# Performance work log

Hardware: AMD Instinct MI355X
Metric: run time of the kernel (lower is better)

Reference implementation:

```python
import jax, jax.numpy as jnp
import numpy as np

HIDDEN = 2048
NUM_HEADS = 16
HEAD_DIM = HIDDEN // NUM_HEADS  # 128
LAYER_IDX = 0


def setup_inputs() -> dict:
    key = jax.random.key(0)
    k1, k2, k3, k4, k5 = jax.random.split(key, 5)
    B, S = 2, 2048
    hidden_states = jax.random.normal(k1, (B, S, HIDDEN), dtype=jnp.float32)
    # causal mask, broadcastable to attn shape (B, Q, H, K)
    causal = jnp.tril(jnp.ones((S, S), dtype=jnp.bool_))  # [Q, K]
    attention_mask = causal[None, :, None, :]  # [1, Q, 1, K]
    c_attn_w = jax.random.normal(k2, (HIDDEN, HIDDEN + 2 * HEAD_DIM), dtype=jnp.float32) * 0.02
    c_attn_b = jax.random.normal(k3, (HIDDEN + 2 * HEAD_DIM,), dtype=jnp.float32) * 0.02
    c_proj_w = jax.random.normal(k4, (HIDDEN, HIDDEN), dtype=jnp.float32) * 0.02
    c_proj_b = jax.random.normal(k5, (HIDDEN,), dtype=jnp.float32) * 0.02
    return {
        "hidden_states": hidden_states,
        "attention_mask": attention_mask,
        "c_attn_w": c_attn_w,
        "c_attn_b": c_attn_b,
        "c_proj_w": c_proj_w,
        "c_proj_b": c_proj_b,
    }


def reference(hidden_states, attention_mask, c_attn_w, c_attn_b, c_proj_w, c_proj_b):
    B, S, D = hidden_states.shape
    H, hd = NUM_HEADS, HEAD_DIM
    # c_attn then split into per-head query and shared (MQA) key/value
    qkv = hidden_states @ c_attn_w + c_attn_b  # [B, S, D + 2*hd]
    query = qkv[..., :D].reshape(B, S, H, hd)  # [B, Q, H, hd]
    k = qkv[..., D:D + hd]                     # [B, K, hd] shared across heads
    v = qkv[..., D + hd:]                      # [B, K, hd]
    # fp32 input => upcast=False => unscale=1, scale = 1/sqrt(head_dim)
    scale = 1.0 / jnp.sqrt(jnp.float32(hd))
    scores = jnp.einsum('bqhd,bkd->bqhk', query, k) * scale  # [B, Q, H, K]
    mask_value = jnp.finfo(jnp.float32).min
    scores = jnp.where(attention_mask, scores, mask_value)
    attn = jax.nn.softmax(scores, axis=-1)
    attn_output = jnp.einsum('bqhk,bkd->bqhd', attn, v).reshape(B, S, D)
    attn_output = attn_output @ c_proj_w + c_proj_b
    return attn_output
```

## Files before the change

### kernel.cpp

```cpp
#include <hip/hip_runtime.h>
#include <hip/hip_bf16.h>

typedef __bf16 bf16_t;
typedef __bf16 bf16x8 __attribute__((ext_vector_type(8)));
typedef __bf16 bf16x4 __attribute__((ext_vector_type(4)));
typedef float f32x4 __attribute__((ext_vector_type(4)));

#define S_LEN 2048
#define HID   2048
#define NH    16
#define HD    128
#define QKVN  2304
#define NEG_BIG (-30000.0f)
#define RESCALE_THR 8.0f

__device__ __forceinline__ void gld_lds16(const bf16_t* g, bf16_t* l) {
  __builtin_amdgcn_global_load_lds(
      (const __attribute__((address_space(1))) void*)((const void*)g),
      (__attribute__((address_space(3))) void*)((void*)l), 16, 0, 0);
}

__global__ __launch_bounds__(256) void cvt_f32_bf16_kernel(
    const float* __restrict__ in, bf16_t* __restrict__ out, int n)
{
  int i = (blockIdx.x * 256 + threadIdx.x) * 4;
  if (i < n) {
    float4 v = *(const float4*)(in + i);
    bf16x4 o;
    o[0] = (bf16_t)v.x; o[1] = (bf16_t)v.y; o[2] = (bf16_t)v.z; o[3] = (bf16_t)v.w;
    *(bf16x4*)(out + i) = o;
  }
}

__global__ __launch_bounds__(256) void transpose_cvt_kernel(
    const float* __restrict__ in, bf16_t* __restrict__ out, int K, int N)
{
  int nc = threadIdx.x & 63;
  int kg = threadIdx.x >> 6;
  int n  = blockIdx.x * 64 + nc;
  int kb = blockIdx.y * 32 + kg * 8;
  bf16x8 v;
  #pragma unroll
  for (int i = 0; i < 8; ++i) v[i] = (bf16_t)in[(size_t)(kb + i) * N + n];
  *(bf16x8*)(out + (size_t)n * K + kb) = v;
}

__global__ __launch_bounds__(256) void vt_extract_kernel(
    const bf16_t* __restrict__ qkv, bf16_t* __restrict__ vtg)
{
  int d  = threadIdx.x & 127;
  int sg = threadIdx.x >> 7;
  int b  = blockIdx.y;
  int s8 = blockIdx.x * 2 + sg;
  bf16x8 v;
  #pragma unroll
  for (int i = 0; i < 8; ++i)
    v[i] = qkv[((size_t)(b * S_LEN + s8 * 8 + i)) * QKVN + HID + HD + d];
  *(bf16x8*)(vtg + ((size_t)(b * HD + d)) * S_LEN + s8 * 8) = v;
}

template <typename OutT>
__global__ __launch_bounds__(512, 4) void gemm_bias_kernel(
    const bf16_t* __restrict__ A, const bf16_t* __restrict__ WT,
    const float* __restrict__ bias, OutT* __restrict__ C,
    int K, int lda, int ldc)
{
  __shared__ bf16_t Ash[2 * 128 * 64];
  __shared__ bf16_t Bsh[2 * 128 * 64];

  const int tid  = threadIdx.x;
  const int wave = tid >> 6;
  const int lane = tid & 63;
  const int quad = lane >> 4;
  const int c16  = lane & 15;
  const int wm = wave >> 2;
  const int wn = wave & 3;

  int id  = (int)(blockIdx.y * gridDim.x + blockIdx.x);
  int nwg = (int)(gridDim.x * gridDim.y);
  int swz = (nwg & 7) ? id : ((id & 7) * (nwg >> 3) + (id >> 3));
  const int n0 = (swz % (int)gridDim.x) * 128;
  const int m0 = (swz / (int)gridDim.x) * 128;

  f32x4 acc[4][2] = {};

  #define GSTAGE(bufi, k0v) do {                                             \
    bf16_t* Ad_ = Ash + (bufi) * 8192;                                       \
    bf16_t* Bd_ = Bsh + (bufi) * 8192;                                       \
    _Pragma("unroll")                                                        \
    for (int j_ = 0; j_ < 2; ++j_) {                                         \
      int cbase_ = wave * 128 + j_ * 64;                                     \
      int c_ = cbase_ + lane;                                                \
      int row_ = c_ >> 3;                                                    \
      int kcl_ = (c_ ^ row_) & 7;                                            \
      gld_lds16(A  + (size_t)(m0 + row_) * lda + (k0v) + kcl_ * 8,           \
                Ad_ + cbase_ * 8);                                           \
      gld_lds16(WT + (size_t)(n0 + row_) * K   + (k0v) + kcl_ * 8,           \
                Bd_ + cbase_ * 8);                                           \
    }                                                                        \
  } while (0)

  GSTAGE(0, 0);
  int cur = 0;

  for (int k0 = 0; k0 < K; k0 += 64) {
    __syncthreads();
    if (k0 + 64 < K) GSTAGE(cur ^ 1, k0 + 64);

    const bf16_t* Ac = Ash + cur * 8192;
    const bf16_t* Bc = Bsh + cur * 8192;
    #pragma unroll
    for (int kk = 0; kk < 2; ++kk) {
      bf16x8 af[4], bfr[2];
      #pragma unroll
      for (int rb = 0; rb < 4; ++rb) {
        int row = wm * 64 + rb * 16 + c16;
        int kcp = ((kk * 4 + quad) ^ row) & 7;
        af[rb] = *(const bf16x8*)(Ac + row * 64 + kcp * 8);
      }
      #pragma unroll
      for (int nt = 0; nt < 2; ++nt) {
        int row = wn * 32 + nt * 16 + c16;
        int kcp = ((kk * 4 + quad) ^ row) & 7;
        bfr[nt] = *(const bf16x8*)(Bc + row * 64 + kcp * 8);
      }
      #pragma unroll
      for (int rb = 0; rb < 4; ++rb)
        #pragma unroll
        for (int nt = 0; nt < 2; ++nt)
          acc[rb][nt] = __builtin_amdgcn_mfma_f32_16x16x32_bf16(af[rb], bfr[nt],
                                                                acc[rb][nt], 0, 0, 0);
    }
    cur ^= 1;
  }
  #undef GSTAGE

  #pragma unroll
  for (int nt = 0; nt < 2; ++nt) {
    int col = n0 + wn * 32 + nt * 16 + c16;
    float bv = bias[col];
    #pragma unroll
    for (int rb = 0; rb < 4; ++rb) {
      int rbase = m0 + wm * 64 + rb * 16 + quad * 4;
      #pragma unroll
      for (int r = 0; r < 4; ++r)
        C[(size_t)(rbase + r) * ldc + col] = (OutT)(acc[rb][nt][r] + bv);
    }
  }
}

__global__ __launch_bounds__(512, 4) void mqa_attn_kernel(
    const bf16_t* __restrict__ qkv, const bf16_t* __restrict__ vtg,
    bf16_t* __restrict__ out)
{
  __shared__ bf16_t sh[40960];

  const int tid  = threadIdx.x;
  const int wv   = tid >> 6;
  const int lane = tid & 63;
  const int quad = lane >> 4;
  const int c16  = lane & 15;
  const int h = blockIdx.y;
  const int b = blockIdx.z;
  const float qscale = 0.08838834764831845f * 1.4426950408889634f;

  const bf16_t* kbase = qkv + (size_t)b * S_LEN * QKVN + HID;
  const bf16_t* vtb   = vtg + (size_t)b * HD * S_LEN;

  const int qh = ((int)blockIdx.x + h) & 15;
  const int Q  = b ? (15 - qh) : qh;
  const int q0 = Q * 128;
  const int qrow = q0 + wv * 16 + c16;
  const int ntile = 2 * Q + 2;

  const bf16_t* qp = qkv + ((size_t)(b * S_LEN + qrow)) * QKVN + h * HD;
  bf16x8 qf[4];
  #pragma unroll
  for (int ks = 0; ks < 4; ++ks) {
    bf16x8 t = *(const bf16x8*)(qp + ks * 32 + quad * 8);
    #pragma unroll
    for (int j = 0; j < 8; ++j) t[j] = (bf16_t)((float)t[j] * qscale);
    qf[ks] = t;
  }

  float m_q = NEG_BIG, l_q = 0.0f;
  f32x4 o[8] = {};

  const int prow = wv * 16 + c16;
  const int rsw  = prow & 7;
  bf16_t* Pbase = sh + 32768 + (size_t)prow * 64;

  #define STAGE(bufi, kti) do {                                              \
    const bf16_t* kb_ = kbase + (size_t)(kti) * 64 * QKVN;                   \
    const bf16_t* vb_ = vtb + (kti) * 64;                                    \
    bf16_t* Kd_ = sh + (bufi) * 8192;                                        \
    bf16_t* Vd_ = sh + 16384 + (bufi) * 8192;                                \
    _Pragma("unroll")                                                        \
    for (int i_ = 0; i_ < 2; ++i_) {                                         \
      int c_ = tid + i_ * 512;                                               \
      int r_ = c_ >> 4, lc_ = (c_ & 15) ^ (r_ & 7);                          \
      gld_lds16(kb_ + (size_t)r_ * QKVN + lc_ * 8, Kd_ + (c_ & ~63) * 8);    \
    }                                                                        \
    _Pragma("unroll")                                                        \
    for (int i_ = 0; i_ < 2; ++i_) {                                         \
      int c_ = tid + i_ * 512;                                               \
      int r_ = c_ >> 3, lc_ = (c_ & 7) ^ (r_ & 7);                           \
      gld_lds16(vb_ + (size_t)r_ * S_LEN + lc_ * 8, Vd_ + (c_ & ~63) * 8);   \
    }                                                                        \
  } while (0)

  STAGE(0, 0);
  int cur = 0;

  for (int kt = 0; kt < ntile; ++kt) {
    __syncthreads();
    if (kt + 1 < ntile) STAGE(cur ^ 1, kt + 1);

    const bf16_t* Kc = sh + cur * 8192;
    const bf16_t* Vc = sh + 16384 + cur * 8192;
    const bool wactive = (kt * 64) <= (q0 + wv * 16 + 15);
    if (wactive) {
      f32x4 sacc[4] = {};
      __builtin_amdgcn_s_setprio(1);
      #pragma unroll
      for (int mt = 0; mt < 4; ++mt) {
        int krow = mt * 16 + c16;
        #pragma unroll
        for (int ks = 0; ks < 4; ++ks) {
          bf16x8 kf = *(const bf16x8*)(Kc + krow * 128 +
                                       (((ks * 4 + quad) ^ (krow & 7)) << 3));
          sacc[mt] = __builtin_amdgcn_mfma_f32_16x16x32_bf16(kf, qf[ks], sacc[mt], 0, 0, 0);
        }
      }
      __builtin_amdgcn_s_setprio(0);

      float mx = NEG_BIG;
      if (kt * 64 + 63 > q0 + wv * 16) {
        #pragma unroll
        for (int mt = 0; mt < 4; ++mt) {
          #pragma unroll
          for (int r = 0; r < 4; ++r) {
            int key = kt * 64 + mt * 16 + quad * 4 + r;
            float v = sacc[mt][r];
            if (key > qrow) v = NEG_BIG;
            sacc[mt][r] = v;
            mx = fmaxf(mx, v);
          }
        }
      } else {
        #pragma unroll
        for (int mt = 0; mt < 4; ++mt) {
          #pragma unroll
          for (int r = 0; r < 4; ++r) mx = fmaxf(mx, sacc[mt][r]);
        }
      }
      mx = fmaxf(mx, __shfl_xor(mx, 16));
      mx = fmaxf(mx, __shfl_xor(mx, 32));

      if (__any(mx > m_q + RESCALE_THR)) {
        float mn = fmaxf(m_q, mx);
        float alpha = __builtin_exp2f(m_q - mn);
        m_q = mn;
        l_q *= alpha;
        #pragma unroll
        for (int mt8 = 0; mt8 < 8; ++mt8) {
          #pragma unroll
          for (int r = 0; r < 4; ++r) o[mt8][r] *= alpha;
        }
      }

      float rs = 0.f;
      #pragma unroll
      for (int mt = 0; mt < 4; ++mt) {
        #pragma unroll
        for (int r = 0; r < 4; ++r) {
          float pe = __builtin_exp2f(sacc[mt][r] - m_q);
          sacc[mt][r] = pe;
          rs += pe;
        }
      }
      rs += __shfl_xor(rs, 16);
      rs += __shfl_xor(rs, 32);
      l_q += rs;

      #pragma unroll
      for (int mt = 0; mt < 4; ++mt) {
        bf16x4 pk;
        #pragma unroll
        for (int r = 0; r < 4; ++r) pk[r] = (bf16_t)sacc[mt][r];
        int ch = 2 * mt + (quad >> 1);
        *(bf16x4*)(Pbase + (((ch ^ rsw) << 3) + (quad & 1) * 4)) = pk;
      }
      bf16x8 pf[2];
      #pragma unroll
      for (int kh = 0; kh < 2; ++kh)
        pf[kh] = *(const bf16x8*)(Pbase + (((4 * kh + quad) ^ rsw) << 3));

      __builtin_amdgcn_s_setprio(1);
      #pragma unroll
      for (int mt8 = 0; mt8 < 8; ++mt8) {
        int vrow = mt8 * 16 + c16;
        #pragma unroll
        for (int kh = 0; kh < 2; ++kh) {
          bf16x8 vf = *(const bf16x8*)(Vc + vrow * 64 +
                                       (((kh * 4 + quad) ^ (vrow & 7)) << 3));
          o[mt8] = __builtin_amdgcn_mfma_f32_16x16x32_bf16(vf, pf[kh], o[mt8], 0, 0, 0);
        }
      }
      __builtin_amdgcn_s_setprio(0);
    }
    cur ^= 1;
  }
  #undef STAGE

  __syncthreads();
  float inv = 1.0f / fmaxf(l_q, 1e-20f);
  bf16_t* Osh = sh;
  #pragma unroll
  for (int mt8 = 0; mt8 < 8; ++mt8) {
    bf16x4 pk;
    #pragma unroll
    for (int r = 0; r < 4; ++r) pk[r] = (bf16_t)(o[mt8][r] * inv);
    *(bf16x4*)(&Osh[(size_t)prow * 136 + mt8 * 16 + quad * 4]) = pk;
  }
  int ql = lane >> 2, dc = lane & 3;
  #pragma unroll
  for (int i = 0; i < 4; ++i) {
    bf16x8 v = *(const bf16x8*)(&Osh[(size_t)(wv * 16 + ql) * 136 + dc * 8 + i * 32]);
    *(bf16x8*)(out + ((size_t)(b * S_LEN + q0 + wv * 16 + ql)) * HID
                   + h * HD + dc * 8 + i * 32) = v;
  }
}

extern "C" void kernel_launch(void* const* d_in, const int* in_sizes, int n_in,
                              void* d_out, int out_size, void* d_ws, size_t ws_size,
                              hipStream_t stream) {
  const float* hidden_f   = (const float*)d_in[0];
  const float* c_attn_w_f = (const float*)d_in[2];
  const float* c_attn_b_f = (const float*)d_in[3];
  const float* c_proj_w_f = (const float*)d_in[4];
  const float* c_proj_b_f = (const float*)d_in[5];
  float* out = (float*)d_out;

  const int M = 2 * S_LEN;
  const int nH  = M * HID;
  const int nWq = HID * QKVN;
  const int nWp = HID * HID;

  bf16_t* hbf   = (bf16_t*)d_ws;
  bf16_t* wqT   = hbf  + nH;
  bf16_t* wpT   = wqT  + nWq;
  bf16_t* qkv   = wpT  + nWp;
  bf16_t* attn  = qkv  + (size_t)M * QKVN;
  bf16_t* vtg   = attn + (size_t)M * HID;

  cvt_f32_bf16_kernel<<<nH / 1024, 256, 0, stream>>>(hidden_f, hbf, nH);
  dim3 gt1(QKVN / 64, HID / 32);
  transpose_cvt_kernel<<<gt1, 256, 0, stream>>>(c_attn_w_f, wqT, HID, QKVN);
  dim3 gt2(HID / 64, HID / 32);
  transpose_cvt_kernel<<<gt2, 256, 0, stream>>>(c_proj_w_f, wpT, HID, HID);

  dim3 g1(QKVN / 128, M / 128);
  gemm_bias_kernel<bf16_t><<<g1, 512, 0, stream>>>(hbf, wqT, c_attn_b_f, qkv,
                                                   HID, HID, QKVN);

  dim3 gv(S_LEN / 16, 2);
  vt_extract_kernel<<<gv, 256, 0, stream>>>(qkv, vtg);

  dim3 g2(16, NH, 2);
  mqa_attn_kernel<<<g2, 512, 0, stream>>>(qkv, vtg, attn);

  dim3 g3(HID / 128, M / 128);
  gemm_bias_kernel<float><<<g3, 512, 0, stream>>>(attn, wpT, c_proj_b_f, out,
                                                  HID, HID, HID);
}
```

Baseline: 300.4 us.

## Merge prep conversions into one kernel and emit V-transpose from QKV GEMM epilogue

```diff
diff --git a/kernel.cpp b/kernel.cpp
--- a/kernel.cpp
+++ b/kernel.cpp
@@ -20,50 +20,47 @@
       (__attribute__((address_space(3))) void*)((void*)l), 16, 0, 0);
 }
 
-__global__ __launch_bounds__(256) void cvt_f32_bf16_kernel(
-    const float* __restrict__ in, bf16_t* __restrict__ out, int n)
+__device__ __forceinline__ void transpose_cvt_body(
+    const float* __restrict__ in, bf16_t* __restrict__ out,
+    int K, int N, int bx, int by, int tid)
 {
-  int i = (blockIdx.x * 256 + threadIdx.x) * 4;
-  if (i < n) {
-    float4 v = *(const float4*)(in + i);
+  int nc = tid & 63;
+  int kg = tid >> 6;
+  int n  = bx * 64 + nc;
+  int kb = by * 32 + kg * 8;
+  bf16x8 v;
+  #pragma unroll
+  for (int i = 0; i < 8; ++i) v[i] = (bf16_t)in[(size_t)(kb + i) * N + n];
+  *(bf16x8*)(out + (size_t)n * K + kb) = v;
+}
+
+__global__ __launch_bounds__(256) void prep_kernel(
+    const float* __restrict__ hidden, bf16_t* __restrict__ hbf,
+    const float* __restrict__ wq, bf16_t* __restrict__ wqT,
+    const float* __restrict__ wp, bf16_t* __restrict__ wpT)
+{
+  const int id  = blockIdx.x;
+  const int tid = threadIdx.x;
+  if (id < 8192) {
+    int i = (id * 256 + tid) * 4;
+    float4 v = *(const float4*)(hidden + i);
     bf16x4 o;
     o[0] = (bf16_t)v.x; o[1] = (bf16_t)v.y; o[2] = (bf16_t)v.z; o[3] = (bf16_t)v.w;
-    *(bf16x4*)(out + i) = o;
-  }
-}
-
-__global__ __launch_bounds__(256) void transpose_cvt_kernel(
-    const float* __restrict__ in, bf16_t* __restrict__ out, int K, int N)
-{
-  int nc = threadIdx.x & 63;
-  int kg = threadIdx.x >> 6;
-  int n  = blockIdx.x * 64 + nc;
-  int kb = blockIdx.y * 32 + kg * 8;
-  bf16x8 v;
-  #pragma unroll
-  for (int i = 0; i < 8; ++i) v[i] = (bf16_t)in[(size_t)(kb + i) * N + n];
-  *(bf16x8*)(out + (size_t)n * K + kb) = v;
-}
-
-__global__ __launch_bounds__(256) void vt_extract_kernel(
-    const bf16_t* __restrict__ qkv, bf16_t* __restrict__ vtg)
-{
-  int d  = threadIdx.x & 127;
-  int sg = threadIdx.x >> 7;
-  int b  = blockIdx.y;
-  int s8 = blockIdx.x * 2 + sg;
-  bf16x8 v;
-  #pragma unroll
-  for (int i = 0; i < 8; ++i)
-    v[i] = qkv[((size_t)(b * S_LEN + s8 * 8 + i)) * QKVN + HID + HD + d];
-  *(bf16x8*)(vtg + ((size_t)(b * HD + d)) * S_LEN + s8 * 8) = v;
+    *(bf16x4*)(hbf + i) = o;
+  } else if (id < 8192 + 2304) {
+    int id2 = id - 8192;
+    transpose_cvt_body(wq, wqT, HID, QKVN, id2 % 36, id2 / 36, tid);
+  } else {
+    int id2 = id - 10496;
+    transpose_cvt_body(wp, wpT, HID, HID, id2 % 32, id2 / 32, tid);
+  }
 }
 
 template <typename OutT>
 __global__ __launch_bounds__(512, 4) void gemm_bias_kernel(
     const bf16_t* __restrict__ A, const bf16_t* __restrict__ WT,
     const float* __restrict__ bias, OutT* __restrict__ C,
-    int K, int lda, int ldc)
+    bf16_t* __restrict__ vt_out, int K, int lda, int ldc)
 {
   __shared__ bf16_t Ash[2 * 128 * 64];
   __shared__ bf16_t Bsh[2 * 128 * 64];
@@ -135,6 +132,7 @@
   }
   #undef GSTAGE
 
+  const bool emit_vt = (vt_out != nullptr) && (n0 == HID + HD);
   #pragma unroll
   for (int nt = 0; nt < 2; ++nt) {
     int col = n0 + wn * 32 + nt * 16 + c16;
@@ -143,8 +141,16 @@
     for (int rb = 0; rb < 4; ++rb) {
       int rbase = m0 + wm * 64 + rb * 16 + quad * 4;
       #pragma unroll
-      for (int r = 0; r < 4; ++r)
-        C[(size_t)(rbase + r) * ldc + col] = (OutT)(acc[rb][nt][r] + bv);
+      for (int r = 0; r < 4; ++r) {
+        float val = acc[rb][nt][r] + bv;
+        int row = rbase + r;
+        C[(size_t)row * ldc + col] = (OutT)val;
+        if (emit_vt) {
+          int d = col - (HID + HD);
+          vt_out[((size_t)(row >> 11) * HD + d) * S_LEN + (row & 2047)] =
+              (bf16_t)val;
+        }
+      }
     }
   }
 }
@@ -354,23 +360,17 @@
   bf16_t* attn  = qkv  + (size_t)M * QKVN;
   bf16_t* vtg   = attn + (size_t)M * HID;
 
-  cvt_f32_bf16_kernel<<<nH / 1024, 256, 0, stream>>>(hidden_f, hbf, nH);
-  dim3 gt1(QKVN / 64, HID / 32);
-  transpose_cvt_kernel<<<gt1, 256, 0, stream>>>(c_attn_w_f, wqT, HID, QKVN);
-  dim3 gt2(HID / 64, HID / 32);
-  transpose_cvt_kernel<<<gt2, 256, 0, stream>>>(c_proj_w_f, wpT, HID, HID);
+  prep_kernel<<<12544, 256, 0, stream>>>(hidden_f, hbf, c_attn_w_f, wqT,
+                                         c_proj_w_f, wpT);
 
   dim3 g1(QKVN / 128, M / 128);
   gemm_bias_kernel<bf16_t><<<g1, 512, 0, stream>>>(hbf, wqT, c_attn_b_f, qkv,
-                                                   HID, HID, QKVN);
-
-  dim3 gv(S_LEN / 16, 2);
-  vt_extract_kernel<<<gv, 256, 0, stream>>>(qkv, vtg);
+                                                   vtg, HID, HID, QKVN);
 
   dim3 g2(16, NH, 2);
   mqa_attn_kernel<<<g2, 512, 0, stream>>>(qkv, vtg, attn);
 
   dim3 g3(HID / 128, M / 128);
   gemm_bias_kernel<float><<<g3, 512, 0, stream>>>(attn, wpT, c_proj_b_f, out,
-                                                  HID, HID, HID);
-}
+                                                  (bf16_t*)nullptr, HID, HID, HID);
+}
```

Result: no change. 300.1 us (-0.1%).
